# Kernel optimization log

Measured on AMD Instinct MI355X. Metric: run time of the kernel, lower is better.

The kernel has to match this reference:

```python
import jax, jax.numpy as jnp
import numpy as np

N_NODES = 50000
N_EDGES = 800000
D_IN = 128
D_SH = 16
D_OUT = 128
N_PATHS = 64


def setup_inputs() -> dict:
    key = jax.random.key(0)
    k1, k2, k3, k4, k5, k6, k7, k8 = jax.random.split(key, 8)
    x = jax.random.normal(k1, (N_NODES, D_IN), dtype=jnp.float32)
    sh = jax.random.normal(k2, (N_EDGES, D_SH), dtype=jnp.float32)
    coeff = jax.random.normal(k3, (N_PATHS,), dtype=jnp.float32)
    src = jax.random.randint(k4, (N_EDGES,), 0, N_NODES, dtype=jnp.int64)
    dst = jax.random.randint(k5, (N_EDGES,), 0, N_NODES, dtype=jnp.int64)
    ki = jax.random.randint(k6, (N_PATHS,), 0, D_IN, dtype=jnp.int32)
    kj = jax.random.randint(k7, (N_PATHS,), 0, D_SH, dtype=jnp.int32)
    ko = jax.random.randint(k8, (N_PATHS,), 0, D_OUT, dtype=jnp.int32)
    return {"x": x, "sh": sh, "coeff": coeff, "src": src, "dst": dst,
            "ki": ki, "kj": kj, "ko": ko}


def reference(x, sh, coeff, src, dst, ki, kj, ko):
    # 1) gather: index_select node features by edge source -> [E, D_in]
    xg = x[src]
    # 2) segmented tensor product: sum over sparse paths p of
    #    coeff[p] * xg[:, ki[p]] * sh[:, kj[p]] accumulated into output slot ko[p]
    vals = coeff[None, :] * xg[:, ki] * sh[:, kj]          # [E, P]
    msg = jnp.zeros((sh.shape[0], D_OUT), dtype=x.dtype).at[:, ko].add(vals)  # [E, D_out]
    # 3) scatter_add messages into per-node output -> [N, D_out]
    out = jnp.zeros((x.shape[0], D_OUT), dtype=x.dtype).at[dst].add(msg)
    return out
```

## Files before the change

kernel.cpp:

```cpp
#include <hip/hip_runtime.h>
#include <hip/hip_fp16.h>

#define N_NODES 50000
#define N_EDGES 800000
#define D_IN    128
#define D_SH    16
#define D_OUT   128
#define N_PATHS 64
#define CAP     64
#define CHUNK   16
#define BLK     256

#define SCAT_T  (N_EDGES / 4)
#define SCAT_B  ((SCAT_T + BLK - 1) / BLK)
#define XC_B    (N_NODES / 16)
#define NODE_B  (N_NODES / 4)

#define OFF_BUK 200000
#define OFF_XCH (OFF_BUK + 25600000)
#define WS_NEED ((size_t)OFF_XCH + 6400000)

__device__ __forceinline__ size_t bslot(int d, int pos) {
    return ((size_t)(pos >> 4) * N_NODES + d) * CHUNK + (pos & 15);
}

__global__ __launch_bounds__(BLK) void build_kernel(
        const float* __restrict__ x, const int* __restrict__ ki,
        const int* __restrict__ src, const int* __restrict__ dst,
        int* __restrict__ cnt, int2* __restrict__ bucket,
        __half* __restrict__ xc_h) {
    if (blockIdx.x < SCAT_B) {
        int idx = blockIdx.x * BLK + threadIdx.x;
        if (idx < SCAT_T) {
            int4 s4 = ((const int4*)src)[idx];
            int4 d4 = ((const int4*)dst)[idx];
            int e0 = idx * 4;
            int p0 = atomicAdd(&cnt[d4.x], 1);
            int p1 = atomicAdd(&cnt[d4.y], 1);
            int p2 = atomicAdd(&cnt[d4.z], 1);
            int p3 = atomicAdd(&cnt[d4.w], 1);
            if (p0 < CAP) bucket[bslot(d4.x, p0)] = make_int2(e0,     s4.x);
            if (p1 < CAP) bucket[bslot(d4.y, p1)] = make_int2(e0 + 1, s4.y);
            if (p2 < CAP) bucket[bslot(d4.z, p2)] = make_int2(e0 + 2, s4.z);
            if (p3 < CAP) bucket[bslot(d4.w, p3)] = make_int2(e0 + 3, s4.w);
        }
    } else {
        const int b2   = blockIdx.x - SCAT_B;
        const int lane = threadIdx.x & 63;
        const int w    = threadIdx.x >> 6;
        const int nb   = b2 * 16 + w * 4;
        const int kil  = ki[lane];
        float x0 = x[(size_t)(nb + 0) * D_IN + kil];
        float x1 = x[(size_t)(nb + 1) * D_IN + kil];
        float x2 = x[(size_t)(nb + 2) * D_IN + kil];
        float x3 = x[(size_t)(nb + 3) * D_IN + kil];
        xc_h[(size_t)(nb + 0) * N_PATHS + lane] = __float2half_rn(x0);
        xc_h[(size_t)(nb + 1) * N_PATHS + lane] = __float2half_rn(x1);
        xc_h[(size_t)(nb + 2) * N_PATHS + lane] = __float2half_rn(x2);
        xc_h[(size_t)(nb + 3) * N_PATHS + lane] = __float2half_rn(x3);
    }
}

__global__ __launch_bounds__(BLK) void node_kernel(
        const float* __restrict__ sh, const __half* __restrict__ xc_h,
        const int* __restrict__ cnt, const int2* __restrict__ bucket,
        const float* __restrict__ coeff, const int* __restrict__ kj,
        const int* __restrict__ ko, float* __restrict__ out) {
    __shared__ float srow[BLK / 64][D_OUT];
    const int lane = threadIdx.x & 63;
    const int w    = threadIdx.x >> 6;
    const int node = blockIdx.x * 4 + w;

    const int   kj_p = kj[lane];
    const int   ko_p = ko[lane];
    const float c_p  = coeff[lane];

    const int cnt_n = __builtin_amdgcn_readfirstlane(min(cnt[node], CAP));

    int e_l = 0, s_l = 0;
    if (lane < cnt_n) {
        int2 pp = bucket[bslot(node, lane)];
        e_l = pp.x; s_l = pp.y;
    }

    float acc = 0.0f;
    int j = 0;
    for (; j + 8 <= cnt_n; j += 8) {
        float xv[8], sv[8];
        #pragma unroll
        for (int u = 0; u < 8; ++u) {
            int e = __builtin_amdgcn_readlane(e_l, j + u);
            int s = __builtin_amdgcn_readlane(s_l, j + u);
            xv[u] = __half2float(xc_h[(size_t)s * N_PATHS + lane]);
            sv[u] = sh[(size_t)e * D_SH + kj_p];
        }
        #pragma unroll
        for (int u = 0; u < 8; ++u) acc += xv[u] * sv[u];
    }
    if (j < cnt_n) {
        float xv[8], sv[8];
        #pragma unroll
        for (int u = 0; u < 8; ++u) {
            int jj = j + u;
            int jc = jj < cnt_n ? jj : 0;
            int e = __builtin_amdgcn_readlane(e_l, jc);
            int s = __builtin_amdgcn_readlane(s_l, jc);
            xv[u] = __half2float(xc_h[(size_t)s * N_PATHS + lane]);
            sv[u] = sh[(size_t)e * D_SH + kj_p];
        }
        #pragma unroll
        for (int u = 0; u < 8; ++u)
            if (j + u < cnt_n) acc += xv[u] * sv[u];
    }
    acc *= c_p;

    srow[w][lane]      = 0.0f;
    srow[w][lane + 64] = 0.0f;
    atomicAdd(&srow[w][ko_p], acc);
    float r0 = srow[w][lane];
    float r1 = srow[w][lane + 64];
    float* orow = out + (size_t)node * D_OUT;
    orow[lane]      = r0;
    orow[lane + 64] = r1;
}

extern "C" void kernel_launch(void* const* d_in, const int* in_sizes, int n_in,
                              void* d_out, int out_size, void* d_ws, size_t ws_size,
                              hipStream_t stream) {
    const float* x     = (const float*)d_in[0];
    const float* sh    = (const float*)d_in[1];
    const float* coeff = (const float*)d_in[2];
    const int*   src   = (const int*)d_in[3];
    const int*   dst   = (const int*)d_in[4];
    const int*   ki    = (const int*)d_in[5];
    const int*   kj    = (const int*)d_in[6];
    const int*   ko    = (const int*)d_in[7];
    float* out = (float*)d_out;

    char* p = (char*)d_ws;
    int*    cnt    = (int*)p;
    int2*   bucket = (int2*)(p + OFF_BUK);
    __half* xc_h   = (__half*)(p + OFF_XCH);
    (void)ws_size;

    hipMemsetAsync(cnt, 0, (size_t)N_NODES * sizeof(int), stream);
    build_kernel<<<SCAT_B + XC_B, BLK, 0, stream>>>(
        x, ki, src, dst, cnt, bucket, xc_h);
    node_kernel<<<NODE_B, BLK, 0, stream>>>(
        sh, xc_h, cnt, bucket, coeff, kj, ko, out);
}
```

Measured before the change: 220.6 us.

## Bin edges by 128-node segments with block-local sort and compact fp16 sh

New measurement: 225.7 us. 1.02x slower.

```diff
diff --git a/kernel.cpp b/kernel.cpp
--- a/kernel.cpp
+++ b/kernel.cpp
@@ -7,47 +7,96 @@
 #define D_SH    16
 #define D_OUT   128
 #define N_PATHS 64
-#define CAP     64
-#define CHUNK   16
+
+#define SEGN    128
+#define NSEG    391
+#define NSEGP   512
+#define CAPE    2560
+#define EPB     3125
+#define BINB    256
+#define XCB     3125
 #define BLK     256
-
-#define SCAT_T  (N_EDGES / 4)
-#define SCAT_B  ((SCAT_T + BLK - 1) / BLK)
-#define XC_B    (N_NODES / 16)
-#define NODE_B  (N_NODES / 4)
-
-#define OFF_BUK 200000
-#define OFF_XCH (OFF_BUK + 25600000)
-#define WS_NEED ((size_t)OFF_XCH + 6400000)
-
-__device__ __forceinline__ size_t bslot(int d, int pos) {
-    return ((size_t)(pos >> 4) * N_NODES + d) * CHUNK + (pos & 15);
-}
-
-__global__ __launch_bounds__(BLK) void build_kernel(
+#define BLK2    512
+
+#define OFF_META 2048
+#define OFF_SH16 (OFF_META + NSEG*CAPE*4)
+#define OFF_XCH  (OFF_SH16 + NSEG*CAPE*32)
+
+__global__ __launch_bounds__(BLK) void bin_kernel(
         const float* __restrict__ x, const int* __restrict__ ki,
-        const int* __restrict__ src, const int* __restrict__ dst,
-        int* __restrict__ cnt, int2* __restrict__ bucket,
+        const float* __restrict__ sh, const int* __restrict__ src,
+        const int* __restrict__ dst, int* __restrict__ segcnt,
+        int* __restrict__ meta, __half* __restrict__ sh16,
         __half* __restrict__ xc_h) {
-    if (blockIdx.x < SCAT_B) {
-        int idx = blockIdx.x * BLK + threadIdx.x;
-        if (idx < SCAT_T) {
-            int4 s4 = ((const int4*)src)[idx];
-            int4 d4 = ((const int4*)dst)[idx];
-            int e0 = idx * 4;
-            int p0 = atomicAdd(&cnt[d4.x], 1);
-            int p1 = atomicAdd(&cnt[d4.y], 1);
-            int p2 = atomicAdd(&cnt[d4.z], 1);
-            int p3 = atomicAdd(&cnt[d4.w], 1);
-            if (p0 < CAP) bucket[bslot(d4.x, p0)] = make_int2(e0,     s4.x);
-            if (p1 < CAP) bucket[bslot(d4.y, p1)] = make_int2(e0 + 1, s4.y);
-            if (p2 < CAP) bucket[bslot(d4.z, p2)] = make_int2(e0 + 2, s4.z);
-            if (p3 < CAP) bucket[bslot(d4.w, p3)] = make_int2(e0 + 3, s4.w);
+    __shared__ int lcnt[NSEGP];
+    __shared__ int lstart[NSEGP];
+    __shared__ int lofs[NSEGP];
+    __shared__ int gbase[NSEGP];
+    __shared__ unsigned short sorted_[EPB];
+    const int tid = threadIdx.x;
+
+    if (blockIdx.x < BINB) {
+        const int e0 = blockIdx.x * EPB;
+        for (int s = tid; s < NSEGP; s += BLK) lcnt[s] = 0;
+        __syncthreads();
+        for (int i = tid; i < EPB; i += BLK)
+            atomicAdd(&lcnt[dst[e0 + i] >> 7], 1);
+        __syncthreads();
+        if (tid < 64) {
+            int b8 = tid * 8, v[8], s0 = 0;
+            #pragma unroll
+            for (int k = 0; k < 8; ++k) { v[k] = lcnt[b8 + k]; s0 += v[k]; }
+            int run = s0;
+            #pragma unroll
+            for (int off = 1; off < 64; off <<= 1) {
+                int y = __shfl_up(run, off);
+                if (tid >= off) run += y;
+            }
+            int acc = run - s0;
+            #pragma unroll
+            for (int k = 0; k < 8; ++k) {
+                lstart[b8 + k] = acc; lofs[b8 + k] = acc; acc += v[k];
+            }
+        } else {
+            for (int s = tid - 64; s < NSEG; s += BLK - 64) {
+                int c = lcnt[s];
+                gbase[s] = c ? atomicAdd(&segcnt[s], c) : 0;
+            }
+        }
+        __syncthreads();
+        for (int i = tid; i < EPB; i += BLK) {
+            int r = atomicAdd(&lofs[dst[e0 + i] >> 7], 1);
+            sorted_[r] = (unsigned short)i;
+        }
+        __syncthreads();
+        for (int j = tid; j < EPB; j += BLK) {
+            int i = sorted_[j];
+            int e = e0 + i;
+            int d = dst[e];
+            int s = d >> 7;
+            int pos = gbase[s] + (j - lstart[s]);
+            if (pos < CAPE) {
+                size_t gi = (size_t)s * CAPE + pos;
+                meta[gi] = src[e] | ((d & 127) << 16);
+                const float4* shv = (const float4*)(sh + (size_t)e * D_SH);
+                float4 f0 = shv[0], f1 = shv[1], f2 = shv[2], f3 = shv[3];
+                union { __half2 h[8]; int4 v[2]; } u;
+                u.h[0] = __floats2half2_rn(f0.x, f0.y);
+                u.h[1] = __floats2half2_rn(f0.z, f0.w);
+                u.h[2] = __floats2half2_rn(f1.x, f1.y);
+                u.h[3] = __floats2half2_rn(f1.z, f1.w);
+                u.h[4] = __floats2half2_rn(f2.x, f2.y);
+                u.h[5] = __floats2half2_rn(f2.z, f2.w);
+                u.h[6] = __floats2half2_rn(f3.x, f3.y);
+                u.h[7] = __floats2half2_rn(f3.z, f3.w);
+                int4* dp = (int4*)(sh16 + gi * 16);
+                dp[0] = u.v[0]; dp[1] = u.v[1];
+            }
         }
     } else {
-        const int b2   = blockIdx.x - SCAT_B;
-        const int lane = threadIdx.x & 63;
-        const int w    = threadIdx.x >> 6;
+        const int b2   = blockIdx.x - BINB;
+        const int lane = tid & 63;
+        const int w    = tid >> 6;
         const int nb   = b2 * 16 + w * 4;
         const int kil  = ki[lane];
         float x0 = x[(size_t)(nb + 0) * D_IN + kil];
@@ -61,67 +110,96 @@
     }
 }
 
-__global__ __launch_bounds__(BLK) void node_kernel(
-        const float* __restrict__ sh, const __half* __restrict__ xc_h,
-        const int* __restrict__ cnt, const int2* __restrict__ bucket,
+__global__ __launch_bounds__(BLK2) void node_kernel(
+        const int* __restrict__ segcnt, const int* __restrict__ meta,
+        const __half* __restrict__ sh16, const __half* __restrict__ xc_h,
         const float* __restrict__ coeff, const int* __restrict__ kj,
         const int* __restrict__ ko, float* __restrict__ out) {
-    __shared__ float srow[BLK / 64][D_OUT];
-    const int lane = threadIdx.x & 63;
-    const int w    = threadIdx.x >> 6;
-    const int node = blockIdx.x * 4 + w;
+    __shared__ int cnt_l[SEGN];
+    __shared__ int nstart[SEGN];
+    __shared__ int ncur[SEGN];
+    __shared__ unsigned short csr[CAPE];
+    __shared__ int metash[CAPE];
+    __shared__ float srow[BLK2 / 64][D_OUT];
+    const int tid  = threadIdx.x;
+    const int lane = tid & 63;
+    const int w    = tid >> 6;
+    const int seg  = blockIdx.x;
+    const int n_e  = min(segcnt[seg], CAPE);
+    const size_t mb = (size_t)seg * CAPE;
+    const __half* shb = sh16 + mb * 16;
+
+    for (int s = tid; s < SEGN; s += BLK2) cnt_l[s] = 0;
+    __syncthreads();
+    for (int i = tid; i < n_e; i += BLK2) {
+        int m = meta[mb + i];
+        metash[i] = m;
+        atomicAdd(&cnt_l[(m >> 16) & 127], 1);
+    }
+    __syncthreads();
+    if (tid < 64) {
+        int b2 = tid * 2;
+        int v0 = cnt_l[b2], v1 = cnt_l[b2 + 1];
+        int s0 = v0 + v1;
+        int run = s0;
+        #pragma unroll
+        for (int off = 1; off < 64; off <<= 1) {
+            int y = __shfl_up(run, off);
+            if (tid >= off) run += y;
+        }
+        int acc = run - s0;
+        nstart[b2] = acc;          ncur[b2] = acc;
+        nstart[b2 + 1] = acc + v0; ncur[b2 + 1] = acc + v0;
+    }
+    __syncthreads();
+    for (int i = tid; i < n_e; i += BLK2) {
+        int dl = (metash[i] >> 16) & 127;
+        int r = atomicAdd(&ncur[dl], 1);
+        csr[r] = (unsigned short)i;
+    }
+    __syncthreads();
 
     const int   kj_p = kj[lane];
     const int   ko_p = ko[lane];
     const float c_p  = coeff[lane];
 
-    const int cnt_n = __builtin_amdgcn_readfirstlane(min(cnt[node], CAP));
-
-    int e_l = 0, s_l = 0;
-    if (lane < cnt_n) {
-        int2 pp = bucket[bslot(node, lane)];
-        e_l = pp.x; s_l = pp.y;
-    }
-
-    float acc = 0.0f;
-    int j = 0;
-    for (; j + 8 <= cnt_n; j += 8) {
-        float xv[8], sv[8];
-        #pragma unroll
-        for (int u = 0; u < 8; ++u) {
-            int e = __builtin_amdgcn_readlane(e_l, j + u);
-            int s = __builtin_amdgcn_readlane(s_l, j + u);
-            xv[u] = __half2float(xc_h[(size_t)s * N_PATHS + lane]);
-            sv[u] = sh[(size_t)e * D_SH + kj_p];
-        }
-        #pragma unroll
-        for (int u = 0; u < 8; ++u) acc += xv[u] * sv[u];
-    }
-    if (j < cnt_n) {
-        float xv[8], sv[8];
-        #pragma unroll
-        for (int u = 0; u < 8; ++u) {
-            int jj = j + u;
-            int jc = jj < cnt_n ? jj : 0;
-            int e = __builtin_amdgcn_readlane(e_l, jc);
-            int s = __builtin_amdgcn_readlane(s_l, jc);
-            xv[u] = __half2float(xc_h[(size_t)s * N_PATHS + lane]);
-            sv[u] = sh[(size_t)e * D_SH + kj_p];
-        }
-        #pragma unroll
-        for (int u = 0; u < 8; ++u)
-            if (j + u < cnt_n) acc += xv[u] * sv[u];
-    }
-    acc *= c_p;
-
-    srow[w][lane]      = 0.0f;
-    srow[w][lane + 64] = 0.0f;
-    atomicAdd(&srow[w][ko_p], acc);
-    float r0 = srow[w][lane];
-    float r1 = srow[w][lane + 64];
-    float* orow = out + (size_t)node * D_OUT;
-    orow[lane]      = r0;
-    orow[lane + 64] = r1;
+    for (int nl = w; nl < SEGN; nl += BLK2 / 64) {
+        const int node = seg * SEGN + nl;
+        if (node >= N_NODES) break;
+        const int st = nstart[nl];
+        const int en = (nl + 1 < SEGN) ? nstart[nl + 1] : n_e;
+        float acc = 0.0f;
+        int j = st;
+        for (; j + 4 <= en; j += 4) {
+            int i0 = csr[j], i1 = csr[j + 1], i2 = csr[j + 2], i3 = csr[j + 3];
+            int m0 = metash[i0], m1 = metash[i1];
+            int m2 = metash[i2], m3 = metash[i3];
+            float x0 = __half2float(xc_h[(size_t)(m0 & 0xFFFF) * N_PATHS + lane]);
+            float s0 = __half2float(shb[(size_t)i0 * 16 + kj_p]);
+            float x1 = __half2float(xc_h[(size_t)(m1 & 0xFFFF) * N_PATHS + lane]);
+            float s1 = __half2float(shb[(size_t)i1 * 16 + kj_p]);
+            float x2 = __half2float(xc_h[(size_t)(m2 & 0xFFFF) * N_PATHS + lane]);
+            float s2 = __half2float(shb[(size_t)i2 * 16 + kj_p]);
+            float x3 = __half2float(xc_h[(size_t)(m3 & 0xFFFF) * N_PATHS + lane]);
+            float s3 = __half2float(shb[(size_t)i3 * 16 + kj_p]);
+            acc += x0 * s0; acc += x1 * s1; acc += x2 * s2; acc += x3 * s3;
+        }
+        for (; j < en; ++j) {
+            int i0 = csr[j];
+            int m0 = metash[i0];
+            acc += __half2float(xc_h[(size_t)(m0 & 0xFFFF) * N_PATHS + lane])
+                 * __half2float(shb[(size_t)i0 * 16 + kj_p]);
+        }
+        acc *= c_p;
+        srow[w][lane]      = 0.0f;
+        srow[w][lane + 64] = 0.0f;
+        atomicAdd(&srow[w][ko_p], acc);
+        float r0 = srow[w][lane];
+        float r1 = srow[w][lane + 64];
+        float* orow = out + (size_t)node * D_OUT;
+        orow[lane]      = r0;
+        orow[lane + 64] = r1;
+    }
 }
 
 extern "C" void kernel_launch(void* const* d_in, const int* in_sizes, int n_in,
@@ -138,14 +216,15 @@
     float* out = (float*)d_out;
 
     char* p = (char*)d_ws;
-    int*    cnt    = (int*)p;
-    int2*   bucket = (int2*)(p + OFF_BUK);
+    int*    segcnt = (int*)p;
+    int*    meta   = (int*)(p + OFF_META);
+    __half* sh16   = (__half*)(p + OFF_SH16);
     __half* xc_h   = (__half*)(p + OFF_XCH);
     (void)ws_size;
 
-    hipMemsetAsync(cnt, 0, (size_t)N_NODES * sizeof(int), stream);
-    build_kernel<<<SCAT_B + XC_B, BLK, 0, stream>>>(
-        x, ki, src, dst, cnt, bucket, xc_h);
-    node_kernel<<<NODE_B, BLK, 0, stream>>>(
-        sh, xc_h, cnt, bucket, coeff, kj, ko, out);
+    hipMemsetAsync(segcnt, 0, 2048, stream);
+    bin_kernel<<<BINB + XCB, BLK, 0, stream>>>(
+        x, ki, sh, src, dst, segcnt, meta, sh16, xc_h);
+    node_kernel<<<NSEG, BLK2, 0, stream>>>(
+        segcnt, meta, sh16, xc_h, coeff, kj, ko, out);
 }
```
